# Optimization experiments

Hardware: AMD Instinct MI355X
Metric: run time of the kernel (lower is better)

The kernel has to match this reference:

```python
import jax, jax.numpy as jnp
import numpy as np
from math import sqrt

B, T, E = 2, 2048, 2048
H, KV, D = 32, 8, 64
R = H // KV  # 4 query heads per kv head


def make_freq_cis(t, d, theta=10000.0):
    # standard rotary table: (T, D/2, 2) holding (cos, sin)
    inv = 1.0 / (theta ** (np.arange(0, d, 2, dtype=np.float32) / d))
    ang = np.arange(t, dtype=np.float32)[:, None] * inv[None, :]
    return jnp.asarray(np.stack([np.cos(ang), np.sin(ang)], axis=-1))


def setup_inputs() -> dict:
    key = jax.random.key(0)
    ks = jax.random.split(key, 5)
    s = 0.02
    return {
        "x": jax.random.normal(ks[0], (B, T, E), dtype=jnp.float32),
        "freq_cis": make_freq_cis(T, D),
        "Wq": jax.random.normal(ks[1], (E, H * D), dtype=jnp.float32) * s,
        "Wk": jax.random.normal(ks[2], (E, KV * D), dtype=jnp.float32) * s,
        "Wv": jax.random.normal(ks[3], (E, KV * D), dtype=jnp.float32) * s,
        "Wo": jax.random.normal(ks[4], (H * D, E), dtype=jnp.float32) * s,
    }


def rope(x, freq_cis):
    # x: (B, T, h, D); complex rotation on adjacent pairs, matching
    # torch view_as_complex(x.reshape(..., D/2, 2)) * freq_cis
    xr = x.reshape(*x.shape[:-1], -1, 2)          # (B,T,h,D/2,2)
    a, b = xr[..., 0], xr[..., 1]
    c = freq_cis[None, :, None, :, 0]             # (1,T,1,D/2)
    s = freq_cis[None, :, None, :, 1]
    out = jnp.stack([a * c - b * s, a * s + b * c], axis=-1)
    return out.reshape(x.shape)


def reference(x, freq_cis, Wq, Wk, Wv, Wo):
    b, t, _ = x.shape
    q = (x @ Wq).reshape(b, t, H, D)
    k = (x @ Wk).reshape(b, t, KV, D)
    v = (x @ Wv).reshape(b, t, KV, D)
    q = rope(q, freq_cis)
    k = rope(k, freq_cis)
    # repeat_interleave kv heads to H (dim=2)
    k = jnp.repeat(k, R, axis=2)
    v = jnp.repeat(v, R, axis=2)
    score = jnp.einsum('bqhd,bkhd->bhqk', q, k) / sqrt(D)
    mask = jnp.tril(jnp.ones((t, t), dtype=bool))
    score = jnp.where(mask[None, None], score, -jnp.inf)
    attn = jax.nn.softmax(score, axis=-1)
    out = jnp.einsum('bhqk,bkhd->bqhd', attn, v).reshape(b, t, H * D)
    return out @ Wo
```

## Files before the change

### kernel.cpp

```cpp
#include <hip/hip_runtime.h>
#include <hip/hip_bf16.h>
#include <math.h>

#define B_   2
#define T_   2048
#define E_   2048
#define H_   32
#define KV_  8
#define D_   64
#define NROW (B_*T_)
#define QW   (H_*D_)
#define KW   (KV_*D_)
#define NQKV 3072

typedef __attribute__((ext_vector_type(8))) short short8;
typedef __attribute__((ext_vector_type(4))) float f32x4;

__device__ __forceinline__ ushort f2bf(float f) {
    __hip_bfloat16 h = __float2bfloat16(f);
    return *reinterpret_cast<ushort*>(&h);
}
__device__ __forceinline__ float bf2f(ushort u) {
    union { unsigned int i; float f; } v; v.i = ((unsigned int)u) << 16; return v.f;
}

__device__ __forceinline__ void gload_lds16(const ushort* g, ushort* l) {
    __builtin_amdgcn_global_load_lds(
        (const __attribute__((address_space(1))) void*)g,
        (__attribute__((address_space(3))) void*)l,
        16, 0, 0);
}

__global__ __launch_bounds__(256)
void cast_bf16(const float* __restrict__ src, ushort* __restrict__ dst)
{
    const size_t i = ((size_t)blockIdx.x * 256 + threadIdx.x) * 8;
    float4 v0 = *reinterpret_cast<const float4*>(src + i);
    float4 v1 = *reinterpret_cast<const float4*>(src + i + 4);
    ushort o[8] = {f2bf(v0.x), f2bf(v0.y), f2bf(v0.z), f2bf(v0.w),
                   f2bf(v1.x), f2bf(v1.y), f2bf(v1.z), f2bf(v1.w)};
    *reinterpret_cast<short8*>(dst + i) = *reinterpret_cast<const short8*>(o);
}

__global__ __launch_bounds__(256)
void transcast(const float* __restrict__ src, ushort* __restrict__ dst, int R, int C)
{
    __shared__ float tile[64][65];
    const int r0 = blockIdx.y * 64, c0 = blockIdx.x * 64;
    const int tid = threadIdx.x;
    const int cc = tid & 63, rb = tid >> 6;
#pragma unroll
    for (int i = 0; i < 16; ++i) {
        int r = rb + i * 4;
        tile[r][cc] = src[(size_t)(r0 + r) * C + c0 + cc];
    }
    __syncthreads();
#pragma unroll
    for (int i = 0; i < 16; ++i) {
        int rr = rb + i * 4;
        dst[(size_t)(c0 + rr) * R + r0 + cc] = f2bf(tile[cc][rr]);
    }
}

template<bool BF16OUT>
__global__ __launch_bounds__(256)
void gemm_bt(const ushort* __restrict__ A, const ushort* __restrict__ BT,
             void* __restrict__ Cv, int N, int K)
{
    __shared__ __align__(16) ushort As[128 * 32];
    __shared__ __align__(16) ushort Bs[128 * 32];
    const int tid = threadIdx.x;
    const int w = tid >> 6, lane = tid & 63;
    const int l15 = lane & 15, g = lane >> 4;
    const int wr = w >> 1, wc = w & 1;
    const size_t brow = (size_t)blockIdx.y * 128, bcol = (size_t)blockIdx.x * 128;

    f32x4 acc[4][4] = {};

    const int srow = w * 32 + (lane >> 2);
    const int skc  = (lane & 3) * 8;
    const ushort* gA = A  + (brow + srow) * K + skc;
    const ushort* gB = BT + (bcol + srow) * K + skc;
    ushort* lA = &As[(w * 32) * 32];
    ushort* lB = &Bs[(w * 32) * 32];

    for (int k0 = 0; k0 < K; k0 += 32) {
        gload_lds16(gA + k0,                  lA);
        gload_lds16(gA + k0 + (size_t)16 * K, lA + 16 * 32);
        gload_lds16(gB + k0,                  lB);
        gload_lds16(gB + k0 + (size_t)16 * K, lB + 16 * 32);
        __syncthreads();

        short8 a[4], b[4];
#pragma unroll
        for (int m = 0; m < 4; ++m)
            a[m] = *reinterpret_cast<const short8*>(&As[(wr * 64 + m * 16 + l15) * 32 + g * 8]);
#pragma unroll
        for (int n = 0; n < 4; ++n)
            b[n] = *reinterpret_cast<const short8*>(&Bs[(wc * 64 + n * 16 + l15) * 32 + g * 8]);
#pragma unroll
        for (int m = 0; m < 4; ++m)
#pragma unroll
            for (int n = 0; n < 4; ++n)
                acc[m][n] = __builtin_amdgcn_mfma_f32_16x16x32_bf16(a[m], b[n], acc[m][n], 0, 0, 0);
        __syncthreads();
    }

#pragma unroll
    for (int m = 0; m < 4; ++m) {
#pragma unroll
        for (int r = 0; r < 4; ++r) {
            const size_t row = brow + wr * 64 + m * 16 + g * 4 + r;
#pragma unroll
            for (int n = 0; n < 4; ++n) {
                const size_t col = bcol + wc * 64 + n * 16 + l15;
                if (BF16OUT) ((ushort*)Cv)[row * N + col] = f2bf(acc[m][n][r]);
                else         ((float*) Cv)[row * N + col] = acc[m][n][r];
            }
        }
    }
}

#define QPAIRS (NROW * H_  * 32)
#define KPAIRS (NROW * KV_ * 32)
#define TPAIRS (QPAIRS + KPAIRS)

__global__ __launch_bounds__(256)
void prep_qk(const ushort* __restrict__ QKVb, const float* __restrict__ fc,
             ushort* __restrict__ Qb, ushort* __restrict__ Kb)
{
    int idx = blockIdx.x * 256 + threadIdx.x;
    if (idx < QPAIRS) {
        int p = idx & 31;
        int t = (idx >> 5) & (T_ - 1);
        int bh = idx >> 16;
        int h = bh & (H_ - 1), b = bh >> 5;
        ushort2 ab = *reinterpret_cast<const ushort2*>(
            QKVb + (size_t)(b * T_ + t) * NQKV + h * 64 + p * 2);
        float c = fc[t * 64 + p * 2], s = fc[t * 64 + p * 2 + 1];
        float x0 = bf2f(ab.x), x1 = bf2f(ab.y);
        ushort2 pk;
        pk.x = f2bf((x0 * c - x1 * s) * 0.125f);
        pk.y = f2bf((x0 * s + x1 * c) * 0.125f);
        *reinterpret_cast<ushort2*>(Qb + (size_t)idx * 2) = pk;
    } else {
        int i2 = idx - QPAIRS;
        int p = i2 & 31;
        int t = (i2 >> 5) & (T_ - 1);
        int bk = i2 >> 16;
        int kh = bk & 7, b = bk >> 3;
        ushort2 ab = *reinterpret_cast<const ushort2*>(
            QKVb + (size_t)(b * T_ + t) * NQKV + 2048 + kh * 64 + p * 2);
        float c = fc[t * 64 + p * 2], s = fc[t * 64 + p * 2 + 1];
        float x0 = bf2f(ab.x), x1 = bf2f(ab.y);
        ushort2 pk;
        pk.x = f2bf(x0 * c - x1 * s);
        pk.y = f2bf(x0 * s + x1 * c);
        *reinterpret_cast<ushort2*>(Kb + (size_t)i2 * 2) = pk;
    }
}

__global__ __launch_bounds__(256)
void transpose_v(const ushort* __restrict__ QKVb, ushort* __restrict__ VT)
{
    __shared__ ushort tile[64][65];
    const int t0 = blockIdx.x * 64;
    const int bk = blockIdx.y;
    const int b = bk >> 3, kh = bk & 7;
    const int tid = threadIdx.x;
    const int c = tid & 63, rbase = tid >> 6;
#pragma unroll
    for (int i = 0; i < 16; ++i) {
        int r = rbase + i * 4;
        tile[r][c] = QKVb[(size_t)(b * T_ + t0 + r) * NQKV + 2560 + kh * 64 + c];
    }
    __syncthreads();
#pragma unroll
    for (int i = 0; i < 16; ++i) {
        int d = rbase + i * 4;
        VT[((size_t)bk * 64 + d) * T_ + t0 + c] = tile[c][d];
    }
}

__device__ __forceinline__
void stage_kv(const ushort* __restrict__ Kh, const ushort* __restrict__ Vh,
              ushort* lK, ushort* lV, int j, int w, int lane)
{
    const int rsub = lane >> 3;
    const int sc   = (lane & 7) ^ rsub;
#pragma unroll
    for (int it = 0; it < 2; ++it) {
        const int row = w * 16 + it * 8 + rsub;
        gload_lds16(Kh + ((size_t)(j * 64 + row)) * 64 + sc * 8,
                    lK + (w * 16 + it * 8) * 64);
        gload_lds16(Vh + (size_t)row * T_ + j * 64 + sc * 8,
                    lV + (w * 16 + it * 8) * 64);
    }
}

#define AQB 128

__global__ __launch_bounds__(256)
void attn_mfma2(const ushort* __restrict__ Qb,
                const ushort* __restrict__ Kb,
                const ushort* __restrict__ VTb,
                ushort* __restrict__ Ob)
{
    __shared__ __align__(16) ushort Ks[2][64 * 64];
    __shared__ __align__(16) ushort Vs[2][64 * 64];
    __shared__ __align__(16) ushort P_lds[4][32 * 64];
    const int qt = (int)gridDim.x - 1 - (int)blockIdx.x;
    const int h = blockIdx.y, b = blockIdx.z;
    const int kvh = h >> 2;
    const int tid = threadIdx.x;
    const int w = tid >> 6, lane = tid & 63;
    const int l15 = lane & 15, g = lane >> 4;

    const ushort* Qh = Qb + (((size_t)b * H_ + h) * T_ + qt * AQB + w * 32) * 64;
    const ushort* Kh = Kb + (((size_t)b * KV_ + kvh) * T_) * 64;
    const ushort* Vh = VTb + ((size_t)b * KV_ + kvh) * 64 * (size_t)T_;

    short8 qf[2][2];
#pragma unroll
    for (int m = 0; m < 2; ++m) {
        qf[m][0] = *reinterpret_cast<const short8*>(Qh + (m * 16 + l15) * 64 + g * 8);
        qf[m][1] = *reinterpret_cast<const short8*>(Qh + (m * 16 + l15) * 64 + 32 + g * 8);
    }

    f32x4 o4[2][4] = {};
    float m_[2][4] = {{-INFINITY, -INFINITY, -INFINITY, -INFINITY},
                      {-INFINITY, -INFINITY, -INFINITY, -INFINITY}};
    float l_[2][4] = {};
    ushort* Pw = P_lds[w];

    const int jend = 2 * qt + 1;
    stage_kv(Kh, Vh, Ks[0], Vs[0], 0, w, lane);
    __syncthreads();

    int cur = 0;
    for (int j = 0; j <= jend; ++j) {
        if (j < jend)
            stage_kv(Kh, Vh, Ks[cur ^ 1], Vs[cur ^ 1], j + 1, w, lane);

        const ushort* Kc = Ks[cur];
        f32x4 s4[2][4] = {};
        __builtin_amdgcn_s_setprio(1);
#pragma unroll
        for (int kk = 0; kk < 2; ++kk) {
            short8 kf[4];
#pragma unroll
            for (int n = 0; n < 4; ++n) {
                const int row = n * 16 + l15;
                kf[n] = *reinterpret_cast<const short8*>(
                    &Kc[row * 64 + (((kk * 4 + g) ^ (row & 7)) << 3)]);
            }
#pragma unroll
            for (int m = 0; m < 2; ++m)
#pragma unroll
                for (int n = 0; n < 4; ++n)
                    s4[m][n] = __builtin_amdgcn_mfma_f32_16x16x32_bf16(qf[m][kk], kf[n], s4[m][n], 0, 0, 0);
        }
        __builtin_amdgcn_s_setprio(0);

        const bool diag = (j >= 2 * qt);
        if (diag) {
#pragma unroll
            for (int m = 0; m < 2; ++m) {
                const int rowq = qt * AQB + w * 32 + m * 16 + g * 4;
#pragma unroll
                for (int n = 0; n < 4; ++n) {
                    const int col = j * 64 + n * 16 + l15;
#pragma unroll
                    for (int r = 0; r < 4; ++r)
                        if (col > rowq + r) s4[m][n][r] = -1e30f;
                }
            }
        }

#pragma unroll
        for (int m = 0; m < 2; ++m)
#pragma unroll
            for (int r = 0; r < 4; ++r) {
                float tmax = fmaxf(fmaxf(s4[m][0][r], s4[m][1][r]),
                                   fmaxf(s4[m][2][r], s4[m][3][r]));
                tmax = fmaxf(tmax, __shfl_xor(tmax, 1));
                tmax = fmaxf(tmax, __shfl_xor(tmax, 2));
                tmax = fmaxf(tmax, __shfl_xor(tmax, 4));
                tmax = fmaxf(tmax, __shfl_xor(tmax, 8));
                const float mn = fmaxf(m_[m][r], tmax);
                const float sc = __expf(m_[m][r] - mn);
                float ps = 0.f;
#pragma unroll
                for (int n = 0; n < 4; ++n) {
                    float p = __expf(s4[m][n][r] - mn);
                    s4[m][n][r] = p;
                    ps += p;
                }
                ps += __shfl_xor(ps, 1);
                ps += __shfl_xor(ps, 2);
                ps += __shfl_xor(ps, 4);
                ps += __shfl_xor(ps, 8);
                l_[m][r] = l_[m][r] * sc + ps;
                m_[m][r] = mn;
#pragma unroll
                for (int n = 0; n < 4; ++n) o4[m][n][r] *= sc;
            }

#pragma unroll
        for (int m = 0; m < 2; ++m)
#pragma unroll
            for (int n = 0; n < 4; ++n)
#pragma unroll
                for (int r = 0; r < 4; ++r) {
                    const int row = m * 16 + g * 4 + r;
                    const int col = n * 16 + l15;
                    Pw[row * 64 + (col ^ ((row & 7) << 3))] = f2bf(s4[m][n][r]);
                }

        const ushort* Vc = Vs[cur];
        __builtin_amdgcn_s_setprio(1);
#pragma unroll
        for (int kk = 0; kk < 2; ++kk) {
            short8 pf[2];
#pragma unroll
            for (int m = 0; m < 2; ++m) {
                const int row = m * 16 + l15;
                pf[m] = *reinterpret_cast<const short8*>(
                    &Pw[row * 64 + (((kk * 4 + g) ^ (row & 7)) << 3)]);
            }
            short8 vf[4];
#pragma unroll
            for (int n = 0; n < 4; ++n) {
                const int row = n * 16 + l15;
                vf[n] = *reinterpret_cast<const short8*>(
                    &Vc[row * 64 + (((kk * 4 + g) ^ (row & 7)) << 3)]);
            }
#pragma unroll
            for (int m = 0; m < 2; ++m)
#pragma unroll
                for (int n = 0; n < 4; ++n)
                    o4[m][n] = __builtin_amdgcn_mfma_f32_16x16x32_bf16(pf[m], vf[n], o4[m][n], 0, 0, 0);
        }
        __builtin_amdgcn_s_setprio(0);

        __syncthreads();
        cur ^= 1;
    }

#pragma unroll
    for (int m = 0; m < 2; ++m)
#pragma unroll
        for (int r = 0; r < 4; ++r) {
            const float inv = 1.f / l_[m][r];
            const int tg = qt * AQB + w * 32 + m * 16 + g * 4 + r;
            ushort* op = Ob + ((size_t)b * T_ + tg) * QW + h * 64;
#pragma unroll
            for (int n = 0; n < 4; ++n)
                op[n * 16 + l15] = f2bf(o4[m][n][r] * inv);
        }
}

extern "C" void kernel_launch(void* const* d_in, const int* in_sizes, int n_in,
                              void* d_out, int out_size, void* d_ws, size_t ws_size,
                              hipStream_t stream)
{
    const float* x  = (const float*)d_in[0];
    const float* fc = (const float*)d_in[1];
    const float* Wq = (const float*)d_in[2];
    const float* Wk = (const float*)d_in[3];
    const float* Wv = (const float*)d_in[4];
    const float* Wo = (const float*)d_in[5];
    float* out = (float*)d_out;

    char* ws = (char*)d_ws;
    ushort* xb   = (ushort*)(ws);
    ushort* WT   = (ushort*)(ws + 16777216);
    ushort* WTo  = (ushort*)(ws + 29360128);
    ushort* QKVb = (ushort*)(ws + 37748736);
    ushort* Qbf  = (ushort*)(ws + 62914560);
    ushort* Kbf  = (ushort*)(ws + 79691776);
    ushort* VT   = (ushort*)(ws + 83886080);
    ushort* Obf  = xb;

    cast_bf16<<<4096, 256, 0, stream>>>(x, xb);
    transcast<<<dim3(32, 32), 256, 0, stream>>>(Wq, WT, E_, QW);
    transcast<<<dim3( 8, 32), 256, 0, stream>>>(Wk, WT + (size_t)2048 * 2048, E_, KW);
    transcast<<<dim3( 8, 32), 256, 0, stream>>>(Wv, WT + (size_t)2560 * 2048, E_, KW);
    transcast<<<dim3(32, 32), 256, 0, stream>>>(Wo, WTo, QW, E_);

    gemm_bt<true><<<dim3(NQKV / 128, NROW / 128), 256, 0, stream>>>(xb, WT, QKVb, NQKV, E_);

    prep_qk<<<TPAIRS / 256, 256, 0, stream>>>(QKVb, fc, Qbf, Kbf);
    transpose_v<<<dim3(T_ / 64, B_ * KV_), 256, 0, stream>>>(QKVb, VT);

    attn_mfma2<<<dim3(T_ / AQB, H_, B_), 256, 0, stream>>>(Qbf, Kbf, VT, Obf);

    gemm_bt<false><<<dim3(E_ / 128, NROW / 128), 256, 0, stream>>>(Obf, WTo, out, E_, E_);
}
```

Measured before the change: 471.8 us.

## Transpose attention MFMA operands so softmax rows are per-lane and skip masked tiles

Swaps the MFMA operand order (K·Q and V·P instead of Q·K and P·V) so each lane holds one query row across the 4 accumulator registers. Row max and sum then need only two cross-lane shuffles instead of four per register, and the probabilities are packed and stored to LDS as 8-byte bf16 pairs. Each wave also skips fully masked KV tiles beyond its own causal limit, and the output is staged through LDS so it can be written to global memory as coalesced 16-byte stores. This adds more indexing complexity and an extra LDS round trip at the end.

```diff
diff --git a/kernel.cpp b/kernel.cpp
--- a/kernel.cpp
+++ b/kernel.cpp
@@ -22,6 +22,9 @@
 }
 __device__ __forceinline__ float bf2f(ushort u) {
     union { unsigned int i; float f; } v; v.i = ((unsigned int)u) << 16; return v.f;
+}
+__device__ __forceinline__ uint pack_bf16(float lo, float hi) {
+    return (uint)f2bf(lo) | ((uint)f2bf(hi) << 16);
 }
 
 __device__ __forceinline__ void gload_lds16(const ushort* g, ushort* l) {
@@ -201,7 +204,7 @@
 #define AQB 128
 
 __global__ __launch_bounds__(256)
-void attn_mfma2(const ushort* __restrict__ Qb,
+void attn_mfma3(const ushort* __restrict__ Qb,
                 const ushort* __restrict__ Kb,
                 const ushort* __restrict__ VTb,
                 ushort* __restrict__ Ob)
@@ -215,6 +218,7 @@
     const int tid = threadIdx.x;
     const int w = tid >> 6, lane = tid & 63;
     const int l15 = lane & 15, g = lane >> 4;
+    const int sw = l15 & 7;
 
     const ushort* Qh = Qb + (((size_t)b * H_ + h) * T_ + qt * AQB + w * 32) * 64;
     const ushort* Kh = Kb + (((size_t)b * KV_ + kvh) * T_) * 64;
@@ -222,17 +226,17 @@
 
     short8 qf[2][2];
 #pragma unroll
-    for (int m = 0; m < 2; ++m) {
-        qf[m][0] = *reinterpret_cast<const short8*>(Qh + (m * 16 + l15) * 64 + g * 8);
-        qf[m][1] = *reinterpret_cast<const short8*>(Qh + (m * 16 + l15) * 64 + 32 + g * 8);
-    }
-
-    f32x4 o4[2][4] = {};
-    float m_[2][4] = {{-INFINITY, -INFINITY, -INFINITY, -INFINITY},
-                      {-INFINITY, -INFINITY, -INFINITY, -INFINITY}};
-    float l_[2][4] = {};
+    for (int nQ = 0; nQ < 2; ++nQ) {
+        qf[nQ][0] = *reinterpret_cast<const short8*>(Qh + (nQ * 16 + l15) * 64 + g * 8);
+        qf[nQ][1] = *reinterpret_cast<const short8*>(Qh + (nQ * 16 + l15) * 64 + 32 + g * 8);
+    }
+
+    f32x4 o4[4][2] = {};
+    float m_[2] = {-INFINITY, -INFINITY};
+    float l_[2] = {0.f, 0.f};
     ushort* Pw = P_lds[w];
 
+    const int qmax_w = qt * AQB + w * 32 + 31;
     const int jend = 2 * qt + 1;
     stage_kv(Kh, Vh, Ks[0], Vs[0], 0, w, lane);
     __syncthreads();
@@ -242,122 +246,143 @@
         if (j < jend)
             stage_kv(Kh, Vh, Ks[cur ^ 1], Vs[cur ^ 1], j + 1, w, lane);
 
-        const ushort* Kc = Ks[cur];
-        f32x4 s4[2][4] = {};
-        __builtin_amdgcn_s_setprio(1);
-#pragma unroll
-        for (int kk = 0; kk < 2; ++kk) {
-            short8 kf[4];
-#pragma unroll
-            for (int n = 0; n < 4; ++n) {
-                const int row = n * 16 + l15;
-                kf[n] = *reinterpret_cast<const short8*>(
-                    &Kc[row * 64 + (((kk * 4 + g) ^ (row & 7)) << 3)]);
-            }
-#pragma unroll
-            for (int m = 0; m < 2; ++m)
-#pragma unroll
-                for (int n = 0; n < 4; ++n)
-                    s4[m][n] = __builtin_amdgcn_mfma_f32_16x16x32_bf16(qf[m][kk], kf[n], s4[m][n], 0, 0, 0);
+        if (j * 64 <= qmax_w) {
+            const ushort* Kc = Ks[cur];
+            f32x4 s4[2][4] = {};
+            __builtin_amdgcn_s_setprio(1);
+#pragma unroll
+            for (int kk = 0; kk < 2; ++kk) {
+                short8 kf[4];
+#pragma unroll
+                for (int mK = 0; mK < 4; ++mK) {
+                    const int row = mK * 16 + l15;
+                    kf[mK] = *reinterpret_cast<const short8*>(
+                        &Kc[row * 64 + (((kk * 4 + g) ^ (row & 7)) << 3)]);
+                }
+#pragma unroll
+                for (int nQ = 0; nQ < 2; ++nQ)
+#pragma unroll
+                    for (int mK = 0; mK < 4; ++mK)
+                        s4[nQ][mK] = __builtin_amdgcn_mfma_f32_16x16x32_bf16(
+                            kf[mK], qf[nQ][kk], s4[nQ][mK], 0, 0, 0);
+            }
+            __builtin_amdgcn_s_setprio(0);
+
+            if (j * 64 + 63 > qt * AQB + w * 32) {
+#pragma unroll
+                for (int nQ = 0; nQ < 2; ++nQ) {
+                    const int qg = qt * AQB + w * 32 + nQ * 16 + l15;
+#pragma unroll
+                    for (int mK = 0; mK < 4; ++mK) {
+                        const int kv0 = j * 64 + mK * 16 + g * 4;
+#pragma unroll
+                        for (int r = 0; r < 4; ++r)
+                            if (kv0 + r > qg) s4[nQ][mK][r] = -1e30f;
+                    }
+                }
+            }
+
+#pragma unroll
+            for (int nQ = 0; nQ < 2; ++nQ) {
+                float tm = fmaxf(fmaxf(fmaxf(s4[nQ][0][0], s4[nQ][0][1]),
+                                       fmaxf(s4[nQ][0][2], s4[nQ][0][3])),
+                                 fmaxf(fmaxf(s4[nQ][1][0], s4[nQ][1][1]),
+                                       fmaxf(s4[nQ][1][2], s4[nQ][1][3])));
+                tm = fmaxf(tm, fmaxf(fmaxf(fmaxf(s4[nQ][2][0], s4[nQ][2][1]),
+                                           fmaxf(s4[nQ][2][2], s4[nQ][2][3])),
+                                     fmaxf(fmaxf(s4[nQ][3][0], s4[nQ][3][1]),
+                                           fmaxf(s4[nQ][3][2], s4[nQ][3][3]))));
+                tm = fmaxf(tm, __shfl_xor(tm, 16));
+                tm = fmaxf(tm, __shfl_xor(tm, 32));
+                const float mn = fmaxf(m_[nQ], tm);
+                const float sc = __expf(m_[nQ] - mn);
+                float ps = 0.f;
+#pragma unroll
+                for (int mK = 0; mK < 4; ++mK) {
+                    float p0 = __expf(s4[nQ][mK][0] - mn);
+                    float p1 = __expf(s4[nQ][mK][1] - mn);
+                    float p2 = __expf(s4[nQ][mK][2] - mn);
+                    float p3 = __expf(s4[nQ][mK][3] - mn);
+                    s4[nQ][mK][0] = p0; s4[nQ][mK][1] = p1;
+                    s4[nQ][mK][2] = p2; s4[nQ][mK][3] = p3;
+                    ps += (p0 + p1) + (p2 + p3);
+                }
+                ps += __shfl_xor(ps, 16);
+                ps += __shfl_xor(ps, 32);
+                l_[nQ] = l_[nQ] * sc + ps;
+                m_[nQ] = mn;
+#pragma unroll
+                for (int mD = 0; mD < 4; ++mD)
+#pragma unroll
+                    for (int r = 0; r < 4; ++r)
+                        o4[mD][nQ][r] *= sc;
+            }
+
+#pragma unroll
+            for (int nQ = 0; nQ < 2; ++nQ) {
+                const int rowi = (nQ * 16 + l15) * 64;
+#pragma unroll
+                for (int mK = 0; mK < 4; ++mK) {
+                    uint2 wv;
+                    wv.x = pack_bf16(s4[nQ][mK][0], s4[nQ][mK][1]);
+                    wv.y = pack_bf16(s4[nQ][mK][2], s4[nQ][mK][3]);
+                    const int idx = rowi + ((((2 * mK + (g >> 1)) ^ sw) << 3) + (g & 1) * 4);
+                    *reinterpret_cast<uint2*>(&Pw[idx]) = wv;
+                }
+            }
+
+            const ushort* Vc = Vs[cur];
+            __builtin_amdgcn_s_setprio(1);
+#pragma unroll
+            for (int kk = 0; kk < 2; ++kk) {
+                short8 pb[2];
+#pragma unroll
+                for (int nQ = 0; nQ < 2; ++nQ)
+                    pb[nQ] = *reinterpret_cast<const short8*>(
+                        &Pw[(nQ * 16 + l15) * 64 + (((4 * kk + g) ^ sw) << 3)]);
+                short8 af[4];
+#pragma unroll
+                for (int mD = 0; mD < 4; ++mD) {
+                    const int row = mD * 16 + l15;
+                    af[mD] = *reinterpret_cast<const short8*>(
+                        &Vc[row * 64 + (((kk * 4 + g) ^ (row & 7)) << 3)]);
+                }
+#pragma unroll
+                for (int mD = 0; mD < 4; ++mD)
+#pragma unroll
+                    for (int nQ = 0; nQ < 2; ++nQ)
+                        o4[mD][nQ] = __builtin_amdgcn_mfma_f32_16x16x32_bf16(
+                            af[mD], pb[nQ], o4[mD][nQ], 0, 0, 0);
+            }
+            __builtin_amdgcn_s_setprio(0);
         }
-        __builtin_amdgcn_s_setprio(0);
-
-        const bool diag = (j >= 2 * qt);
-        if (diag) {
-#pragma unroll
-            for (int m = 0; m < 2; ++m) {
-                const int rowq = qt * AQB + w * 32 + m * 16 + g * 4;
-#pragma unroll
-                for (int n = 0; n < 4; ++n) {
-                    const int col = j * 64 + n * 16 + l15;
-#pragma unroll
-                    for (int r = 0; r < 4; ++r)
-                        if (col > rowq + r) s4[m][n][r] = -1e30f;
-                }
-            }
-        }
-
-#pragma unroll
-        for (int m = 0; m < 2; ++m)
-#pragma unroll
-            for (int r = 0; r < 4; ++r) {
-                float tmax = fmaxf(fmaxf(s4[m][0][r], s4[m][1][r]),
-                                   fmaxf(s4[m][2][r], s4[m][3][r]));
-                tmax = fmaxf(tmax, __shfl_xor(tmax, 1));
-                tmax = fmaxf(tmax, __shfl_xor(tmax, 2));
-                tmax = fmaxf(tmax, __shfl_xor(tmax, 4));
-                tmax = fmaxf(tmax, __shfl_xor(tmax, 8));
-                const float mn = fmaxf(m_[m][r], tmax);
-                const float sc = __expf(m_[m][r] - mn);
-                float ps = 0.f;
-#pragma unroll
-                for (int n = 0; n < 4; ++n) {
-                    float p = __expf(s4[m][n][r] - mn);
-                    s4[m][n][r] = p;
-                    ps += p;
-                }
-                ps += __shfl_xor(ps, 1);
-                ps += __shfl_xor(ps, 2);
-                ps += __shfl_xor(ps, 4);
-                ps += __shfl_xor(ps, 8);
-                l_[m][r] = l_[m][r] * sc + ps;
-                m_[m][r] = mn;
-#pragma unroll
-                for (int n = 0; n < 4; ++n) o4[m][n][r] *= sc;
-            }
-
-#pragma unroll
-        for (int m = 0; m < 2; ++m)
-#pragma unroll
-            for (int n = 0; n < 4; ++n)
-#pragma unroll
-                for (int r = 0; r < 4; ++r) {
-                    const int row = m * 16 + g * 4 + r;
-                    const int col = n * 16 + l15;
-                    Pw[row * 64 + (col ^ ((row & 7) << 3))] = f2bf(s4[m][n][r]);
-                }
-
-        const ushort* Vc = Vs[cur];
-        __builtin_amdgcn_s_setprio(1);
-#pragma unroll
-        for (int kk = 0; kk < 2; ++kk) {
-            short8 pf[2];
-#pragma unroll
-            for (int m = 0; m < 2; ++m) {
-                const int row = m * 16 + l15;
-                pf[m] = *reinterpret_cast<const short8*>(
-                    &Pw[row * 64 + (((kk * 4 + g) ^ (row & 7)) << 3)]);
-            }
-            short8 vf[4];
-#pragma unroll
-            for (int n = 0; n < 4; ++n) {
-                const int row = n * 16 + l15;
-                vf[n] = *reinterpret_cast<const short8*>(
-                    &Vc[row * 64 + (((kk * 4 + g) ^ (row & 7)) << 3)]);
-            }
-#pragma unroll
-            for (int m = 0; m < 2; ++m)
-#pragma unroll
-                for (int n = 0; n < 4; ++n)
-                    o4[m][n] = __builtin_amdgcn_mfma_f32_16x16x32_bf16(pf[m], vf[n], o4[m][n], 0, 0, 0);
-        }
-        __builtin_amdgcn_s_setprio(0);
 
         __syncthreads();
         cur ^= 1;
     }
 
-#pragma unroll
-    for (int m = 0; m < 2; ++m)
-#pragma unroll
-        for (int r = 0; r < 4; ++r) {
-            const float inv = 1.f / l_[m][r];
-            const int tg = qt * AQB + w * 32 + m * 16 + g * 4 + r;
-            ushort* op = Ob + ((size_t)b * T_ + tg) * QW + h * 64;
-#pragma unroll
-            for (int n = 0; n < 4; ++n)
-                op[n * 16 + l15] = f2bf(o4[m][n][r] * inv);
+    const float inv[2] = {1.f / l_[0], 1.f / l_[1]};
+#pragma unroll
+    for (int nQ = 0; nQ < 2; ++nQ) {
+        const int rowi = (nQ * 16 + l15) * 64;
+#pragma unroll
+        for (int mD = 0; mD < 4; ++mD) {
+            uint2 wv;
+            wv.x = pack_bf16(o4[mD][nQ][0] * inv[nQ], o4[mD][nQ][1] * inv[nQ]);
+            wv.y = pack_bf16(o4[mD][nQ][2] * inv[nQ], o4[mD][nQ][3] * inv[nQ]);
+            const int idx = rowi + ((((2 * mD + (g >> 1)) ^ sw) << 3) + (g & 1) * 4);
+            *reinterpret_cast<uint2*>(&Pw[idx]) = wv;
         }
+    }
+#pragma unroll
+    for (int p4 = 0; p4 < 4; ++p4) {
+        const int q2 = p4 * 8 + (lane >> 3);
+        const int c  = lane & 7;
+        short8 v = *reinterpret_cast<const short8*>(
+            &Pw[q2 * 64 + (((c ^ (q2 & 7)) << 3))]);
+        const int qg = qt * AQB + w * 32 + q2;
+        *reinterpret_cast<short8*>(Ob + ((size_t)b * T_ + qg) * QW + h * 64 + c * 8) = v;
+    }
 }
 
 extern "C" void kernel_launch(void* const* d_in, const int* in_sizes, int n_in,
@@ -393,7 +418,7 @@
     prep_qk<<<TPAIRS / 256, 256, 0, stream>>>(QKVb, fc, Qbf, Kbf);
     transpose_v<<<dim3(T_ / 64, B_ * KV_), 256, 0, stream>>>(QKVb, VT);
 
-    attn_mfma2<<<dim3(T_ / AQB, H_, B_), 256, 0, stream>>>(Qbf, Kbf, VT, Obf);
+    attn_mfma3<<<dim3(T_ / AQB, H_, B_), 256, 0, stream>>>(Qbf, Kbf, VT, Obf);
 
     gemm_bt<false><<<dim3(E_ / 128, NROW / 128), 256, 0, stream>>>(Obf, WTo, out, E_, E_);
 }
```

New measurement: 406.4 us. 13.9% less time.
